# Kernel optimization log

Measured on AMD Instinct MI355X. Metric: run time of the kernel, lower is better.

The kernel has to match this reference:

```python
import jax, jax.numpy as jnp
import numpy as np

D = 512; E = 8; TOPK = 2; F = 2048; H = 4
SF_LEVELS = 4; SF_BASE = 4.0; LN_EPS = 1e-5


def _ln(h, s, b):
    mu = jnp.mean(h, axis=-1, keepdims=True)
    var = jnp.mean((h - mu) ** 2, axis=-1, keepdims=True)
    return (h - mu) / jnp.sqrt(var + LN_EPS) * s + b


def setup_inputs() -> dict:
    key = jax.random.key(0)
    ks = jax.random.split(key, 16)
    sc = 0.02
    inp = {
        "x": jax.random.normal(ks[0], (4, 1024, D), jnp.float32),
        "gate_w": jax.random.normal(ks[1], (D, E), jnp.float32) * sc,
        "gate_b": jnp.zeros((E,), jnp.float32),
        "ln1_s": jnp.ones((E, D), jnp.float32),
        "ln1_b": jnp.zeros((E, D), jnp.float32),
        "ln2_s": jnp.ones((E, D), jnp.float32),
        "ln2_b": jnp.zeros((E, D), jnp.float32),
        "wq": jax.random.normal(ks[2], (E, D, D), jnp.float32) * sc,
        "wk": jax.random.normal(ks[3], (E, D, D), jnp.float32) * sc,
        "wv": jax.random.normal(ks[4], (E, D, D), jnp.float32) * sc,
        "wo": jax.random.normal(ks[5], (E, D, D), jnp.float32) * sc,
        "bq": jnp.zeros((E, D), jnp.float32),
        "bk": jnp.zeros((E, D), jnp.float32),
        "bv": jnp.zeros((E, D), jnp.float32),
        "bo": jnp.zeros((E, D), jnp.float32),
        "w1": jax.random.normal(ks[6], (E, D, F), jnp.float32) * sc,
        "b1": jnp.zeros((E, F), jnp.float32),
        "w2": jax.random.normal(ks[7], (E, F, D), jnp.float32) * sc,
        "b2": jnp.zeros((E, D), jnp.float32),
    }
    return inp


def reference(x, gate_w, gate_b, ln1_s, ln1_b, ln2_s, ln2_b, wq, wk, wv, wo, bq, bk, bv, bo, w1, b1, w2, b2):
    B, S, d = x.shape
    dh = d // H
    # --- SpikingRouter ---
    logits = x @ gate_w + gate_b                       # [B,S,E]
    _, idx = jax.lax.top_k(logits, TOPK)               # [B,S,k]
    in_topk = jnp.sum(jax.nn.one_hot(idx, E, dtype=logits.dtype), axis=-2) > 0
    routing_in = jnp.where(in_topk, jax.nn.relu(logits), 0.0)
    # Scale-and-Fire neuron: multi-level threshold quantization
    mem = routing_in
    rw = jnp.zeros_like(mem)
    for lvl in range(SF_LEVELS):
        thr = SF_BASE / (2.0 ** lvl)
        spk = (mem >= thr).astype(mem.dtype)
        rw = rw + spk * thr
        mem = mem - spk * thr
    # --- all experts (SFormerBlock, post-norm transformer block) ---
    def block(p):
        l1s, l1b, l2s, l2b, Wq, Wk, Wv, Wo, Bq, Bk, Bv, Bo, W1, B1, W2, B2 = p
        q = (x @ Wq + Bq).reshape(B, S, H, dh)
        k = (x @ Wk + Bk).reshape(B, S, H, dh)
        v = (x @ Wv + Bv).reshape(B, S, H, dh)
        scores = jnp.einsum('bqhd,bkhd->bhqk', q, k) / jnp.sqrt(jnp.asarray(dh, x.dtype))
        att = jax.nn.softmax(scores, axis=-1)
        o = jnp.einsum('bhqk,bkhd->bqhd', att, v).reshape(B, S, d) @ Wo + Bo
        h = _ln(x + o, l1s, l1b)
        f = jax.nn.relu(h @ W1 + B1) @ W2 + B2
        return _ln(h + f, l2s, l2b)

    expert_outs = jax.vmap(block)((ln1_s, ln1_b, ln2_s, ln2_b, wq, wk, wv, wo, bq, bk, bv, bo, w1, b1, w2, b2))  # [E,B,S,D]
    final = jnp.einsum('ebsd,bse->bsd', expert_outs, rw)
    return final, logits
```

## Files before the change

kernel.cpp:

```cpp
#include <hip/hip_runtime.h>
#include <hip/hip_bf16.h>
#include <stdint.h>

using u16 = unsigned short;
typedef float floatx4 __attribute__((ext_vector_type(4)));
typedef __bf16 bfv8 __attribute__((ext_vector_type(8)));

#define AS1 __attribute__((address_space(1)))
#define AS3 __attribute__((address_space(3)))

__device__ __forceinline__ u16 f2bf_bits(float f) {
    __hip_bfloat16 h = __float2bfloat16(f);
    u16 u;
    __builtin_memcpy(&u, &h, 2);
    return u;
}
__device__ __forceinline__ float bf_bits2f(u16 u) {
    __hip_bfloat16 h;
    __builtin_memcpy(&h, &u, 2);
    return __bfloat162float(h);
}
__device__ __forceinline__ void gload_lds16(const void* g, void* l) {
    __builtin_amdgcn_global_load_lds((AS1 void*)(uintptr_t)g, (AS3 void*)l, 16, 0, 0);
}

__device__ __forceinline__ void stage64(const u16* __restrict__ Abase, long lda, const long* arow,
                                        const u16* __restrict__ Bb, long ldb, int k0, int tid,
                                        u16* Ad, u16* Bd) {
    #pragma unroll
    for (int j = 0; j < 4; ++j) {
        const int q   = j * 256 + tid;
        const int row = q >> 3;
        const int cg  = (q & 7) ^ (row & 7);
        gload_lds16(Abase + arow[j] * lda + k0 + cg * 8, Ad + q * 8);
        gload_lds16(Bb + (long)row * ldb + k0 + cg * 8, Bd + q * 8);
    }
}
__device__ __forceinline__ void compute64(const u16* Ab, const u16* Bb, int wy, int wx,
                                          int quad, int mrow, floatx4 acc[4][4]) {
    #pragma unroll
    for (int kk = 0; kk < 2; ++kk) {
        bfv8 af[4], bf[4];
        #pragma unroll
        for (int mi = 0; mi < 4; mi++) {
            const int r = wy * 64 + mi * 16 + mrow;
            const int slot = (kk * 4 + quad) ^ (r & 7);
            af[mi] = *(const bfv8*)&Ab[r * 64 + slot * 8];
        }
        #pragma unroll
        for (int ni = 0; ni < 4; ni++) {
            const int r = wx * 64 + ni * 16 + mrow;
            const int slot = (kk * 4 + quad) ^ (r & 7);
            bf[ni] = *(const bfv8*)&Bb[r * 64 + slot * 8];
        }
        #pragma unroll
        for (int mi = 0; mi < 4; mi++)
            #pragma unroll
            for (int ni = 0; ni < 4; ni++)
                acc[mi][ni] = __builtin_amdgcn_mfma_f32_16x16x32_bf16(af[mi], bf[ni], acc[mi][ni], 0, 0, 0);
    }
}

__global__ void cast_bf16_kernel(const float* __restrict__ in, u16* __restrict__ out, int n4) {
    int i = blockIdx.x * blockDim.x + threadIdx.x;
    if (i >= n4) return;
    float4 v = ((const float4*)in)[i];
    ushort4 o;
    o.x = f2bf_bits(v.x); o.y = f2bf_bits(v.y); o.z = f2bf_bits(v.z); o.w = f2bf_bits(v.w);
    ((ushort4*)out)[i] = o;
}

__global__ void transpose_cast_kernel(const float* __restrict__ src, u16* __restrict__ dst,
                                      int R, int C, long sSrc, long sDst) {
    __shared__ float tile[32][33];
    const float* s = src + (long)blockIdx.z * sSrc;
    u16* d = dst + (long)blockIdx.z * sDst;
    int c0 = blockIdx.x * 32, r0 = blockIdx.y * 32;
    int tx = threadIdx.x, ty = threadIdx.y;
    #pragma unroll
    for (int i = 0; i < 4; i++)
        tile[ty + 8*i][tx] = s[(long)(r0 + ty + 8*i) * C + c0 + tx];
    __syncthreads();
    #pragma unroll
    for (int i = 0; i < 4; i++)
        d[(long)(c0 + ty + 8*i) * R + r0 + tx] = f2bf_bits(tile[tx][ty + 8*i]);
}

__global__ void pack_bias_kernel(const float* __restrict__ bq, const float* __restrict__ bk,
                                 const float* __restrict__ bv, float* __restrict__ pb) {
    int i = blockIdx.x * 256 + threadIdx.x;
    const float* s = blockIdx.y == 0 ? bq : (blockIdx.y == 1 ? bk : bv);
    pb[blockIdx.y * 4096 + i] = s[i];
}

__global__ __launch_bounds__(512)
void router_kernel(const float* __restrict__ x, const float* __restrict__ gw,
                   const float* __restrict__ gb, float* __restrict__ rw,
                   float* __restrict__ logits_out) {
    int row = blockIdx.x;
    int w = threadIdx.x >> 6;
    int lane = threadIdx.x & 63;
    const float* xr = x + (long)row * 512;
    float sum = 0.f;
    #pragma unroll
    for (int i = 0; i < 8; i++) {
        int d = lane + 64 * i;
        sum += xr[d] * gw[d * 8 + w];
    }
    #pragma unroll
    for (int o = 32; o; o >>= 1) sum += __shfl_down(sum, o, 64);
    __shared__ float lg[8];
    if (lane == 0) lg[w] = sum + gb[w];
    __syncthreads();
    if (threadIdx.x == 0) {
        float l[8];
        #pragma unroll
        for (int e = 0; e < 8; e++) l[e] = lg[e];
        int i1 = 0;
        for (int e = 1; e < 8; e++) if (l[e] > l[i1]) i1 = e;
        int i2 = -1;
        for (int e = 0; e < 8; e++) { if (e == i1) continue; if (i2 < 0 || l[e] > l[i2]) i2 = e; }
        for (int e = 0; e < 8; e++) {
            float v = (e == i1 || e == i2) ? (l[e] > 0.f ? l[e] : 0.f) : 0.f;
            float r = 0.f, mem = v;
            #pragma unroll
            for (int lvl = 0; lvl < 4; lvl++) {
                float thr = 4.0f / (float)(1 << lvl);
                if (mem >= thr) { r += thr; mem -= thr; }
            }
            rw[(long)row * 8 + e] = r;
            logits_out[(long)row * 8 + e] = l[e];
        }
    }
}

__global__ __launch_bounds__(256)
void build_lists_kernel(const float* __restrict__ rw, int* __restrict__ prix,
                        int* __restrict__ act, int* __restrict__ smap,
                        int* __restrict__ tmap, int* __restrict__ tt, int* __restrict__ pt) {
    int b = blockIdx.x;
    int t = threadIdx.x, wv = t >> 6, lane = t & 63;
    __shared__ int wsum[4];
    __shared__ int base_sh;
    if (t == 0) base_sh = 0;
    __syncthreads();
    for (int e = 0; e < 8; e++) {
        int r0 = b * 1024 + t * 4;
        int f[4], c = 0;
        #pragma unroll
        for (int i = 0; i < 4; i++) {
            f[i] = (rw[(long)(r0 + i) * 8 + e] != 0.f) ? 1 : 0;
            c += f[i];
        }
        int incl = c;
        #pragma unroll
        for (int o = 1; o < 64; o <<= 1) {
            int n = __shfl_up(incl, o, 64);
            if (lane >= o) incl += n;
        }
        if (lane == 63) wsum[wv] = incl;
        __syncthreads();
        int woff = 0;
        #pragma unroll
        for (int k = 0; k < 4; k++) if (k < wv) woff += wsum[k];
        int tot = wsum[0] + wsum[1] + wsum[2] + wsum[3];
        int excl = incl - c + woff;
        int base = base_sh;
        int slot = excl;
        #pragma unroll
        for (int i = 0; i < 4; i++) {
            int r = r0 + i;
            if (f[i]) {
                int ps = base + slot;
                prix[b * 3072 + ps] = r;
                act[b * 3072 + ps] = 1;
                smap[(long)r * 8 + e] = ps;
                slot++;
            } else {
                smap[(long)r * 8 + e] = -1;
            }
        }
        int pad = (tot + 127) & ~127;
        for (int s = tot + t; s < pad; s += 256) {
            prix[b * 3072 + base + s] = b * 1024;
            act[b * 3072 + base + s] = 0;
        }
        for (int k = t; k < (pad >> 7); k += 256)
            tmap[b * 32 + (base >> 7) + k] = e;
        __syncthreads();
        if (t == 0) base_sh = base + pad;
        __syncthreads();
    }
    if (t == 0) {
        tt[b] = base_sh >> 7;
        pt[b] = base_sh;
    }
}

template<bool TRANSC>
__global__ __launch_bounds__(256)
void gemm_dense_kernel(const u16* __restrict__ A,
                       const u16* __restrict__ B, long sB,
                       u16* __restrict__ C, long sC,
                       const float* __restrict__ bias, int K) {
    __shared__ __align__(16) u16 As[2][128 * 64];
    __shared__ __align__(16) u16 Bs[2][128 * 64];
    const int z = blockIdx.z;
    const u16* Bb = B + (long)z * sB + (long)blockIdx.x * 128 * 512;

    const int tid = threadIdx.x;
    const int w = tid >> 6, lane = tid & 63;
    const int wy = w >> 1, wx = w & 1;
    const int quad = lane >> 4, mrow = lane & 15;

    long arow[4];
    #pragma unroll
    for (int j = 0; j < 4; ++j) arow[j] = (long)blockIdx.y * 128 + ((j * 256 + tid) >> 3);

    floatx4 acc[4][4];
    #pragma unroll
    for (int i = 0; i < 4; i++)
        #pragma unroll
        for (int j = 0; j < 4; j++)
            acc[i][j] = floatx4{0.f, 0.f, 0.f, 0.f};

    const int nk = K >> 6;
    stage64(A, 512, arow, Bb, 512, 0, tid, As[0], Bs[0]);
    for (int it = 0; it < nk; ++it) {
        const int cur = it & 1;
        __syncthreads();
        if (it + 1 < nk)
            stage64(A, 512, arow, Bb, 512, (it + 1) << 6, tid, As[1 - cur], Bs[1 - cur]);
        compute64(As[cur], Bs[cur], wy, wx, quad, mrow, acc);
    }

    const float* biasb = bias + (long)z * 512 + blockIdx.x * 128;
    if constexpr (TRANSC) {
        u16* Cb = C + (long)z * sC;
        #pragma unroll
        for (int ni = 0; ni < 4; ni++) {
            const int colt = wx * 64 + ni * 16 + mrow;
            const int n = blockIdx.x * 128 + colt;
            float bv = biasb[colt];
            #pragma unroll
            for (int mi = 0; mi < 4; mi++) {
                #pragma unroll
                for (int r = 0; r < 4; r++) {
                    const int m = blockIdx.y * 128 + wy * 64 + mi * 16 + quad * 4 + r;
                    float v = acc[mi][ni][r] + bv;
                    long addr = ((long)(((m >> 10) << 2) + (n >> 7)) * 128 + (n & 127)) * 1024 + (m & 1023);
                    Cb[addr] = f2bf_bits(v);
                }
            }
        }
    } else {
        u16* Cb = C + (long)z * sC + (long)blockIdx.y * 128 * 512 + blockIdx.x * 128;
        #pragma unroll
        for (int ni = 0; ni < 4; ni++) {
            const int col = wx * 64 + ni * 16 + mrow;
            float bv = biasb[col];
            #pragma unroll
            for (int mi = 0; mi < 4; mi++) {
                #pragma unroll
                for (int r = 0; r < 4; r++) {
                    const int row = wy * 64 + mi * 16 + quad * 4 + r;
                    Cb[(long)row * 512 + col] = f2bf_bits(acc[mi][ni][r] + bv);
                }
            }
        }
    }
}

__global__ __launch_bounds__(256)
void gemm_scores_kernel(const u16* __restrict__ Q, const u16* __restrict__ Km, u16* __restrict__ S,
                        const int* __restrict__ prix, const int* __restrict__ tmap,
                        const int* __restrict__ tt, float alpha) {
    const int b = blockIdx.z >> 2, h = blockIdx.z & 3;
    const int tile = blockIdx.y;
    if (tile >= tt[b]) return;
    const int e = tmap[b * 32 + tile];
    __shared__ __align__(16) u16 As[2][128 * 64];
    __shared__ __align__(16) u16 Bs[2][128 * 64];
    const u16* Abase = Q + (long)e * 4096 * 512 + h * 128;
    const u16* Bb = Km + ((long)e * 4096 + b * 1024 + blockIdx.x * 128) * 512 + h * 128;

    const int tid = threadIdx.x;
    const int w = tid >> 6, lane = tid & 63;
    const int wy = w >> 1, wx = w & 1;
    const int quad = lane >> 4, mrow = lane & 15;

    long arow[4];
    #pragma unroll
    for (int j = 0; j < 4; ++j)
        arow[j] = prix[b * 3072 + tile * 128 + ((j * 256 + tid) >> 3)];

    floatx4 acc[4][4];
    #pragma unroll
    for (int i = 0; i < 4; i++)
        #pragma unroll
        for (int j = 0; j < 4; j++)
            acc[i][j] = floatx4{0.f, 0.f, 0.f, 0.f};

    stage64(Abase, 512, arow, Bb, 512, 0, tid, As[0], Bs[0]);
    for (int it = 0; it < 2; ++it) {
        const int cur = it & 1;
        __syncthreads();
        if (it == 0)
            stage64(Abase, 512, arow, Bb, 512, 64, tid, As[1], Bs[1]);
        compute64(As[cur], Bs[cur], wy, wx, quad, mrow, acc);
    }

    u16* Cb = S + ((long)blockIdx.z * 3072 + tile * 128) * 1024 + blockIdx.x * 128;
    #pragma unroll
    for (int ni = 0; ni < 4; ni++) {
        const int col = wx * 64 + ni * 16 + mrow;
        #pragma unroll
        for (int mi = 0; mi < 4; mi++) {
            #pragma unroll
            for (int r = 0; r < 4; r++) {
                const int row = wy * 64 + mi * 16 + quad * 4 + r;
                Cb[(long)row * 1024 + col] = f2bf_bits(acc[mi][ni][r] * alpha);
            }
        }
    }
}

__global__ __launch_bounds__(256)
void gemm_pv_kernel(const u16* __restrict__ S, const u16* __restrict__ VT, u16* __restrict__ OC,
                    const int* __restrict__ tmap, const int* __restrict__ tt) {
    const int b = blockIdx.z >> 2, h = blockIdx.z & 3;
    const int tile = blockIdx.y;
    if (tile >= tt[b]) return;
    const int e = tmap[b * 32 + tile];
    __shared__ __align__(16) u16 As[2][128 * 64];
    __shared__ __align__(16) u16 Bs[2][128 * 64];
    const u16* Abase = S + ((long)blockIdx.z * 3072 + tile * 128) * 1024;
    const u16* Bb = VT + ((long)e * 16 + blockIdx.z) * 131072;

    const int tid = threadIdx.x;
    const int w = tid >> 6, lane = tid & 63;
    const int wy = w >> 1, wx = w & 1;
    const int quad = lane >> 4, mrow = lane & 15;

    long arow[4];
    #pragma unroll
    for (int j = 0; j < 4; ++j) arow[j] = (j * 256 + tid) >> 3;

    floatx4 acc[4][4];
    #pragma unroll
    for (int i = 0; i < 4; i++)
        #pragma unroll
        for (int j = 0; j < 4; j++)
            acc[i][j] = floatx4{0.f, 0.f, 0.f, 0.f};

    stage64(Abase, 1024, arow, Bb, 1024, 0, tid, As[0], Bs[0]);
    for (int it = 0; it < 16; ++it) {
        const int cur = it & 1;
        __syncthreads();
        if (it + 1 < 16)
            stage64(Abase, 1024, arow, Bb, 1024, (it + 1) << 6, tid, As[1 - cur], Bs[1 - cur]);
        compute64(As[cur], Bs[cur], wy, wx, quad, mrow, acc);
    }

    u16* Cb = OC + ((long)b * 3072 + tile * 128) * 512 + h * 128;
    #pragma unroll
    for (int ni = 0; ni < 4; ni++) {
        const int col = wx * 64 + ni * 16 + mrow;
        #pragma unroll
        for (int mi = 0; mi < 4; mi++) {
            #pragma unroll
            for (int r = 0; r < 4; r++) {
                const int row = wy * 64 + mi * 16 + quad * 4 + r;
                Cb[(long)row * 512 + col] = f2bf_bits(acc[mi][ni][r]);
            }
        }
    }
}

template<bool RELU>
__global__ __launch_bounds__(256)
void gemm_packed_kernel(const u16* __restrict__ A, int lda,
                        const u16* __restrict__ B, int ldb, long sBe,
                        u16* __restrict__ C, int ldc,
                        const float* __restrict__ bias, long sBiasE,
                        const int* __restrict__ tmap, const int* __restrict__ tt, int K) {
    const int b = blockIdx.y / 24, tile = blockIdx.y % 24;
    if (tile >= tt[b]) return;
    const int e = tmap[b * 32 + tile];
    __shared__ __align__(16) u16 As[2][128 * 64];
    __shared__ __align__(16) u16 Bs[2][128 * 64];
    const long rbase = (long)b * 3072 + tile * 128;
    const u16* Ab = A + rbase * lda;
    const u16* Bb = B + (long)e * sBe + (long)blockIdx.x * 128 * ldb;

    const int tid = threadIdx.x;
    const int w = tid >> 6, lane = tid & 63;
    const int wy = w >> 1, wx = w & 1;
    const int quad = lane >> 4, mrow = lane & 15;

    long arow[4];
    #pragma unroll
    for (int j = 0; j < 4; ++j) arow[j] = (j * 256 + tid) >> 3;

    floatx4 acc[4][4];
    #pragma unroll
    for (int i = 0; i < 4; i++)
        #pragma unroll
        for (int j = 0; j < 4; j++)
            acc[i][j] = floatx4{0.f, 0.f, 0.f, 0.f};

    const int nk = K >> 6;
    stage64(Ab, lda, arow, Bb, ldb, 0, tid, As[0], Bs[0]);
    for (int it = 0; it < nk; ++it) {
        const int cur = it & 1;
        __syncthreads();
        if (it + 1 < nk)
            stage64(Ab, lda, arow, Bb, ldb, (it + 1) << 6, tid, As[1 - cur], Bs[1 - cur]);
        compute64(As[cur], Bs[cur], wy, wx, quad, mrow, acc);
    }

    u16* Cb = C + rbase * ldc + (long)blockIdx.x * 128;
    const float* biasb = bias + (long)e * sBiasE + blockIdx.x * 128;
    #pragma unroll
    for (int ni = 0; ni < 4; ni++) {
        const int col = wx * 64 + ni * 16 + mrow;
        float bv = biasb[col];
        #pragma unroll
        for (int mi = 0; mi < 4; mi++) {
            #pragma unroll
            for (int r = 0; r < 4; r++) {
                const int row = wy * 64 + mi * 16 + quad * 4 + r;
                float v = acc[mi][ni][r] + bv;
                if (RELU) v = fmaxf(v, 0.f);
                Cb[(long)row * ldc + col] = f2bf_bits(v);
            }
        }
    }
}

__global__ __launch_bounds__(256)
void softmax_kernel(u16* __restrict__ S, const int* __restrict__ act, const int* __restrict__ pt) {
    int blk = blockIdx.x;
    int pslot = blk % 3072;
    int bh = blk / 3072;
    int b = bh >> 2;
    if (pslot >= pt[b] || !act[b * 3072 + pslot]) return;
    u16* p = S + ((long)bh * 3072 + pslot) * 1024;
    int t = threadIdx.x, w = t >> 6, lane = t & 63;
    float v[4];
    float mx = -1e30f;
    #pragma unroll
    for (int i = 0; i < 4; i++) {
        v[i] = bf_bits2f(p[t + 256 * i]);
        mx = fmaxf(mx, v[i]);
    }
    #pragma unroll
    for (int o = 32; o; o >>= 1) mx = fmaxf(mx, __shfl_down(mx, o, 64));
    __shared__ float red[8];
    if (lane == 0) red[w] = mx;
    __syncthreads();
    mx = fmaxf(fmaxf(red[0], red[1]), fmaxf(red[2], red[3]));
    float sum = 0.f;
    #pragma unroll
    for (int i = 0; i < 4; i++) { v[i] = __expf(v[i] - mx); sum += v[i]; }
    #pragma unroll
    for (int o = 32; o; o >>= 1) sum += __shfl_down(sum, o, 64);
    if (lane == 0) red[4 + w] = sum;
    __syncthreads();
    float inv = 1.f / (red[4] + red[5] + red[6] + red[7]);
    #pragma unroll
    for (int i = 0; i < 4; i++) p[t + 256 * i] = f2bf_bits(v[i] * inv);
}

__global__ __launch_bounds__(128)
void ln1_kernel(const float* __restrict__ x, const u16* __restrict__ tc,
                const int* __restrict__ prix, const int* __restrict__ act,
                const int* __restrict__ tmap, const int* __restrict__ pt,
                const float* __restrict__ s_all, const float* __restrict__ b_all,
                u16* __restrict__ hb) {
    int blk = blockIdx.x;
    int b = blk / 3072, pslot = blk % 3072;
    if (pslot >= pt[b]) return;
    long row = (long)b * 3072 + pslot;
    int tid = threadIdx.x, w = tid >> 6, lane = tid & 63;
    if (!act[row]) {
        *(ushort4*)(hb + row * 512 + tid * 4) = make_ushort4(0, 0, 0, 0);
        return;
    }
    int r = prix[row];
    int e = tmap[b * 32 + (pslot >> 7)];
    float4 xv = *(const float4*)(x + (long)r * 512 + tid * 4);
    ushort4 tu = *(const ushort4*)(tc + row * 512 + tid * 4);
    float v[4] = {xv.x + bf_bits2f(tu.x), xv.y + bf_bits2f(tu.y),
                  xv.z + bf_bits2f(tu.z), xv.w + bf_bits2f(tu.w)};
    float sum = v[0] + v[1] + v[2] + v[3];
    #pragma unroll
    for (int o = 32; o; o >>= 1) sum += __shfl_down(sum, o, 64);
    __shared__ float sh[4];
    if (lane == 0) sh[w] = sum;
    __syncthreads();
    float mu = (sh[0] + sh[1]) * (1.f / 512.f);
    float sq = 0.f;
    #pragma unroll
    for (int j = 0; j < 4; j++) { float d = v[j] - mu; sq += d * d; }
    #pragma unroll
    for (int o = 32; o; o >>= 1) sq += __shfl_down(sq, o, 64);
    if (lane == 0) sh[2 + w] = sq;
    __syncthreads();
    float inv = 1.f / sqrtf((sh[2] + sh[3]) * (1.f / 512.f) + 1e-5f);
    float4 sv = *(const float4*)(s_all + e * 512 + tid * 4);
    float4 bv = *(const float4*)(b_all + e * 512 + tid * 4);
    ushort4 ub;
    ub.x = f2bf_bits((v[0] - mu) * inv * sv.x + bv.x);
    ub.y = f2bf_bits((v[1] - mu) * inv * sv.y + bv.y);
    ub.z = f2bf_bits((v[2] - mu) * inv * sv.z + bv.z);
    ub.w = f2bf_bits((v[3] - mu) * inv * sv.w + bv.w);
    *(ushort4*)(hb + row * 512 + tid * 4) = ub;
}

__global__ __launch_bounds__(128)
void ln2acc_kernel(const u16* __restrict__ hb, const u16* __restrict__ t2,
                   const float* __restrict__ s_all, const float* __restrict__ b_all,
                   const float* __restrict__ rw, const int* __restrict__ smap,
                   float* __restrict__ out) {
    long r = blockIdx.x;
    int b = (int)(r >> 10);
    int tid = threadIdx.x, w = tid >> 6, lane = tid & 63;
    __shared__ float sh[4];
    float4 acc = make_float4(0.f, 0.f, 0.f, 0.f);
    for (int e = 0; e < 8; e++) {
        int ps = smap[r * 8 + e];
        if (ps >= 0) {
            float wgt = rw[r * 8 + e];
            long row = (long)b * 3072 + ps;
            ushort4 hu = *(const ushort4*)(hb + row * 512 + tid * 4);
            ushort4 fu = *(const ushort4*)(t2 + row * 512 + tid * 4);
            float v[4] = {bf_bits2f(hu.x) + bf_bits2f(fu.x), bf_bits2f(hu.y) + bf_bits2f(fu.y),
                          bf_bits2f(hu.z) + bf_bits2f(fu.z), bf_bits2f(hu.w) + bf_bits2f(fu.w)};
            float sum = v[0] + v[1] + v[2] + v[3];
            #pragma unroll
            for (int o = 32; o; o >>= 1) sum += __shfl_down(sum, o, 64);
            if (lane == 0) sh[w] = sum;
            __syncthreads();
            float mu = (sh[0] + sh[1]) * (1.f / 512.f);
            float sq = 0.f;
            #pragma unroll
            for (int j = 0; j < 4; j++) { float d = v[j] - mu; sq += d * d; }
            #pragma unroll
            for (int o = 32; o; o >>= 1) sq += __shfl_down(sq, o, 64);
            if (lane == 0) sh[2 + w] = sq;
            __syncthreads();
            float inv = 1.f / sqrtf((sh[2] + sh[3]) * (1.f / 512.f) + 1e-5f);
            float4 sv = *(const float4*)(s_all + e * 512 + tid * 4);
            float4 bv = *(const float4*)(b_all + e * 512 + tid * 4);
            acc.x += wgt * ((v[0] - mu) * inv * sv.x + bv.x);
            acc.y += wgt * ((v[1] - mu) * inv * sv.y + bv.y);
            acc.z += wgt * ((v[2] - mu) * inv * sv.z + bv.z);
            acc.w += wgt * ((v[3] - mu) * inv * sv.w + bv.w);
            __syncthreads();
        }
    }
    *(float4*)(out + r * 512 + tid * 4) = acc;
}

static const size_t WB_B   = 0;
static const size_t RW_B   = 50331648;
static const size_t PB_B   = 50462720;
static const size_t TT_B   = 50511872;
static const size_t PT_B   = 50511888;
static const size_t TMAP_B = 50511904;
static const size_t PRIX_B = 50512416;
static const size_t ACT_B  = 50561568;
static const size_t SMAP_B = 50610720;
static const size_t XB_B   = 50741792;
static const size_t Q8_B   = 54936096;
static const size_t K8_B   = 88490528;
static const size_t VT_B   = 122044960;
static const size_t S_B    = 155599392;
static const size_t OC_B   = Q8_B;
static const size_t TC_B   = K8_B;
static const size_t HB_B   = Q8_B;
static const size_t MID_B  = S_B;
static const size_t T2_B   = VT_B;

extern "C" void kernel_launch(void* const* d_in, const int* in_sizes, int n_in,
                              void* d_out, int out_size, void* d_ws, size_t ws_size,
                              hipStream_t stream) {
    const float* x      = (const float*)d_in[0];
    const float* gate_w = (const float*)d_in[1];
    const float* gate_b = (const float*)d_in[2];
    const float* ln1_s  = (const float*)d_in[3];
    const float* ln1_b  = (const float*)d_in[4];
    const float* ln2_s  = (const float*)d_in[5];
    const float* ln2_b  = (const float*)d_in[6];
    const float* wq = (const float*)d_in[7];
    const float* wk = (const float*)d_in[8];
    const float* wv = (const float*)d_in[9];
    const float* wo = (const float*)d_in[10];
    const float* bo = (const float*)d_in[14];
    const float* w1 = (const float*)d_in[15];
    const float* b1 = (const float*)d_in[16];
    const float* w2 = (const float*)d_in[17];
    const float* b2 = (const float*)d_in[18];
    float* out = (float*)d_out;

    char* ws = (char*)d_ws;
    u16*   WB   = (u16*)(ws + WB_B);
    float* RW   = (float*)(ws + RW_B);
    float* PB   = (float*)(ws + PB_B);
    int*   TT   = (int*)(ws + TT_B);
    int*   PT   = (int*)(ws + PT_B);
    int*   TMAP = (int*)(ws + TMAP_B);
    int*   PRIX = (int*)(ws + PRIX_B);
    int*   ACT  = (int*)(ws + ACT_B);
    int*   SMAP = (int*)(ws + SMAP_B);
    u16*   XB   = (u16*)(ws + XB_B);
    u16*   Q8   = (u16*)(ws + Q8_B);
    u16*   VT8  = (u16*)(ws + VT_B);
    u16*   S    = (u16*)(ws + S_B);
    u16*   K8   = (u16*)(ws + K8_B);
    u16*   OC   = (u16*)(ws + OC_B);
    u16*   TC   = (u16*)(ws + TC_B);
    u16*   HB   = (u16*)(ws + HB_B);
    u16*   MID  = (u16*)(ws + MID_B);
    u16*   T2   = (u16*)(ws + T2_B);

    cast_bf16_kernel<<<dim3(2048), 256, 0, stream>>>(x, XB, 4096 * 512 / 4);
    transpose_cast_kernel<<<dim3(16,16,8), dim3(32,8), 0, stream>>>(wq, WB + 0,        512,  512,  262144,  262144);
    transpose_cast_kernel<<<dim3(16,16,8), dim3(32,8), 0, stream>>>(wk, WB + 2097152,  512,  512,  262144,  262144);
    transpose_cast_kernel<<<dim3(16,16,8), dim3(32,8), 0, stream>>>(wv, WB + 4194304,  512,  512,  262144,  262144);
    transpose_cast_kernel<<<dim3(16,16,8), dim3(32,8), 0, stream>>>(wo, WB + 6291456,  512,  512,  262144,  262144);
    transpose_cast_kernel<<<dim3(64,16,8), dim3(32,8), 0, stream>>>(w1, WB + 8388608,  512,  2048, 1048576, 1048576);
    transpose_cast_kernel<<<dim3(16,64,8), dim3(32,8), 0, stream>>>(w2, WB + 16777216, 2048, 512,  1048576, 1048576);
    pack_bias_kernel<<<dim3(16,3), 256, 0, stream>>>((const float*)d_in[11], (const float*)d_in[12],
                                                     (const float*)d_in[13], PB);
    router_kernel<<<4096, 512, 0, stream>>>(x, gate_w, gate_b, RW, out + 2097152);
    build_lists_kernel<<<4, 256, 0, stream>>>(RW, PRIX, ACT, SMAP, TMAP, TT, PT);

    const float isq = 0.08838834764831845f;

    gemm_dense_kernel<false><<<dim3(4,32,16), 256, 0, stream>>>(
        XB, WB, 262144, Q8, 2097152, PB, 512);
    gemm_dense_kernel<true><<<dim3(4,32,8), 256, 0, stream>>>(
        XB, WB + 4194304, 262144, VT8, 2097152, PB + 8192, 512);

    gemm_scores_kernel<<<dim3(8,24,16), 256, 0, stream>>>(
        Q8, K8, S, PRIX, TMAP, TT, isq);
    softmax_kernel<<<49152, 256, 0, stream>>>(S, ACT, PT);
    gemm_pv_kernel<<<dim3(1,24,16), 256, 0, stream>>>(S, VT8, OC, TMAP, TT);

    gemm_packed_kernel<false><<<dim3(4,96), 256, 0, stream>>>(
        OC, 512, WB + 6291456, 512, 262144, TC, 512, bo, 512, TMAP, TT, 512);
    ln1_kernel<<<12288, 128, 0, stream>>>(x, TC, PRIX, ACT, TMAP, PT, ln1_s, ln1_b, HB);
    gemm_packed_kernel<true><<<dim3(16,96), 256, 0, stream>>>(
        HB, 512, WB + 8388608, 512, 1048576, MID, 2048, b1, 2048, TMAP, TT, 512);
    gemm_packed_kernel<false><<<dim3(4,96), 256, 0, stream>>>(
        MID, 2048, WB + 16777216, 2048, 1048576, T2, 512, b2, 512, TMAP, TT, 2048);
    ln2acc_kernel<<<4096, 128, 0, stream>>>(HB, T2, ln2_s, ln2_b, RW, SMAP, out);
}
```

Before: 502.9 us.

## Fuse softmax into score GEMM epilogue and compute Q only for routed tokens

Removes the standalone softmax kernel. The scores GEMM now applies exp in its epilogue and writes per-tile row partial sums, and the PV GEMM normalises its output by the reciprocal of the summed partials. Q projection changes from a dense GEMM over all tokens for every expert to a gathered packed GEMM over only the routed rows. The weight transpose launches and the bias pack are also merged into fewer kernels. Exp is taken without max subtraction, which risks overflow for large scores, and a new partial-sum buffer is added to the workspace.

Measured after the change: 477.0 us. 5.1% less time.

```diff
diff --git a/kernel.cpp b/kernel.cpp
--- a/kernel.cpp
+++ b/kernel.cpp
@@ -61,7 +61,15 @@
     }
 }
 
-__global__ void cast_bf16_kernel(const float* __restrict__ in, u16* __restrict__ out, int n4) {
+__global__ void cast_bf16_kernel(const float* __restrict__ in, u16* __restrict__ out, int n4,
+                                 const float* __restrict__ bq, const float* __restrict__ bk,
+                                 const float* __restrict__ bv, float* __restrict__ pb) {
+    if (blockIdx.x >= 2048) {
+        int j = (blockIdx.x - 2048) * 256 + threadIdx.x;
+        const float* s = j < 4096 ? bq : (j < 8192 ? bk : bv);
+        pb[j] = s[j & 4095];
+        return;
+    }
     int i = blockIdx.x * blockDim.x + threadIdx.x;
     if (i >= n4) return;
     float4 v = ((const float4*)in)[i];
@@ -86,11 +94,22 @@
         d[(long)(c0 + ty + 8*i) * R + r0 + tx] = f2bf_bits(tile[tx][ty + 8*i]);
 }
 
-__global__ void pack_bias_kernel(const float* __restrict__ bq, const float* __restrict__ bk,
-                                 const float* __restrict__ bv, float* __restrict__ pb) {
-    int i = blockIdx.x * 256 + threadIdx.x;
-    const float* s = blockIdx.y == 0 ? bq : (blockIdx.y == 1 ? bk : bv);
-    pb[blockIdx.y * 4096 + i] = s[i];
+__global__ void transpose_cast4_kernel(const float* __restrict__ w0, const float* __restrict__ w1p,
+                                       const float* __restrict__ w2p, const float* __restrict__ w3p,
+                                       u16* __restrict__ dst) {
+    __shared__ float tile[32][33];
+    int z = blockIdx.z;
+    const float* s = (z < 8 ? w0 : z < 16 ? w1p : z < 24 ? w2p : w3p) + (long)(z & 7) * 262144;
+    u16* d = dst + (long)z * 262144;
+    int c0 = blockIdx.x * 32, r0 = blockIdx.y * 32;
+    int tx = threadIdx.x, ty = threadIdx.y;
+    #pragma unroll
+    for (int i = 0; i < 4; i++)
+        tile[ty + 8*i][tx] = s[(long)(r0 + ty + 8*i) * 512 + c0 + tx];
+    __syncthreads();
+    #pragma unroll
+    for (int i = 0; i < 4; i++)
+        d[(long)(c0 + ty + 8*i) * 512 + r0 + tx] = f2bf_bits(tile[tx][ty + 8*i]);
 }
 
 __global__ __launch_bounds__(512)
@@ -272,16 +291,17 @@
 }
 
 __global__ __launch_bounds__(256)
-void gemm_scores_kernel(const u16* __restrict__ Q, const u16* __restrict__ Km, u16* __restrict__ S,
-                        const int* __restrict__ prix, const int* __restrict__ tmap,
-                        const int* __restrict__ tt, float alpha) {
+void gemm_scores_kernel(const u16* __restrict__ QP, const u16* __restrict__ Km, u16* __restrict__ S,
+                        const int* __restrict__ tmap, const int* __restrict__ tt,
+                        float* __restrict__ psum, float alpha) {
     const int b = blockIdx.z >> 2, h = blockIdx.z & 3;
     const int tile = blockIdx.y;
     if (tile >= tt[b]) return;
     const int e = tmap[b * 32 + tile];
     __shared__ __align__(16) u16 As[2][128 * 64];
     __shared__ __align__(16) u16 Bs[2][128 * 64];
-    const u16* Abase = Q + (long)e * 4096 * 512 + h * 128;
+    __shared__ float psh[2][128];
+    const u16* Abase = QP + (long)b * 3072 * 512 + h * 128;
     const u16* Bb = Km + ((long)e * 4096 + b * 1024 + blockIdx.x * 128) * 512 + h * 128;
 
     const int tid = threadIdx.x;
@@ -292,7 +312,7 @@
     long arow[4];
     #pragma unroll
     for (int j = 0; j < 4; ++j)
-        arow[j] = prix[b * 3072 + tile * 128 + ((j * 256 + tid) >> 3)];
+        arow[j] = tile * 128 + ((j * 256 + tid) >> 3);
 
     floatx4 acc[4][4];
     #pragma unroll
@@ -310,6 +330,28 @@
         compute64(As[cur], Bs[cur], wy, wx, quad, mrow, acc);
     }
 
+    #pragma unroll
+    for (int mi = 0; mi < 4; mi++) {
+        #pragma unroll
+        for (int r = 0; r < 4; r++) {
+            float s = 0.f;
+            #pragma unroll
+            for (int ni = 0; ni < 4; ni++) {
+                float p = __expf(acc[mi][ni][r] * alpha);
+                acc[mi][ni][r] = p;
+                s += p;
+            }
+            #pragma unroll
+            for (int o = 1; o < 16; o <<= 1) s += __shfl_xor(s, o, 64);
+            if (mrow == 0) psh[wx][wy * 64 + mi * 16 + quad * 4 + r] = s;
+        }
+    }
+    __syncthreads();
+    if (tid < 128) {
+        long prow = (long)blockIdx.z * 3072 + tile * 128 + tid;
+        psum[prow * 8 + blockIdx.x] = psh[0][tid] + psh[1][tid];
+    }
+
     u16* Cb = S + ((long)blockIdx.z * 3072 + tile * 128) * 1024 + blockIdx.x * 128;
     #pragma unroll
     for (int ni = 0; ni < 4; ni++) {
@@ -319,7 +361,7 @@
             #pragma unroll
             for (int r = 0; r < 4; r++) {
                 const int row = wy * 64 + mi * 16 + quad * 4 + r;
-                Cb[(long)row * 1024 + col] = f2bf_bits(acc[mi][ni][r] * alpha);
+                Cb[(long)row * 1024 + col] = f2bf_bits(acc[mi][ni][r]);
             }
         }
     }
@@ -327,13 +369,15 @@
 
 __global__ __launch_bounds__(256)
 void gemm_pv_kernel(const u16* __restrict__ S, const u16* __restrict__ VT, u16* __restrict__ OC,
-                    const int* __restrict__ tmap, const int* __restrict__ tt) {
+                    const int* __restrict__ tmap, const int* __restrict__ tt,
+                    const float* __restrict__ psum) {
     const int b = blockIdx.z >> 2, h = blockIdx.z & 3;
     const int tile = blockIdx.y;
     if (tile >= tt[b]) return;
     const int e = tmap[b * 32 + tile];
     __shared__ __align__(16) u16 As[2][128 * 64];
     __shared__ __align__(16) u16 Bs[2][128 * 64];
+    __shared__ float invs[128];
     const u16* Abase = S + ((long)blockIdx.z * 3072 + tile * 128) * 1024;
     const u16* Bb = VT + ((long)e * 16 + blockIdx.z) * 131072;
 
@@ -341,6 +385,14 @@
     const int w = tid >> 6, lane = tid & 63;
     const int wy = w >> 1, wx = w & 1;
     const int quad = lane >> 4, mrow = lane & 15;
+
+    if (tid < 128) {
+        const float* ps = psum + ((long)blockIdx.z * 3072 + tile * 128 + tid) * 8;
+        float s = 0.f;
+        #pragma unroll
+        for (int i = 0; i < 8; i++) s += ps[i];
+        invs[tid] = 1.f / s;
+    }
 
     long arow[4];
     #pragma unroll
@@ -371,26 +423,27 @@
             #pragma unroll
             for (int r = 0; r < 4; r++) {
                 const int row = wy * 64 + mi * 16 + quad * 4 + r;
-                Cb[(long)row * 512 + col] = f2bf_bits(acc[mi][ni][r]);
-            }
-        }
-    }
-}
-
-template<bool RELU>
+                Cb[(long)row * 512 + col] = f2bf_bits(acc[mi][ni][r] * invs[row]);
+            }
+        }
+    }
+}
+
+template<bool RELU, bool GATHER>
 __global__ __launch_bounds__(256)
 void gemm_packed_kernel(const u16* __restrict__ A, int lda,
                         const u16* __restrict__ B, int ldb, long sBe,
                         u16* __restrict__ C, int ldc,
                         const float* __restrict__ bias, long sBiasE,
-                        const int* __restrict__ tmap, const int* __restrict__ tt, int K) {
+                        const int* __restrict__ tmap, const int* __restrict__ tt, int K,
+                        const int* __restrict__ prix) {
     const int b = blockIdx.y / 24, tile = blockIdx.y % 24;
     if (tile >= tt[b]) return;
     const int e = tmap[b * 32 + tile];
     __shared__ __align__(16) u16 As[2][128 * 64];
     __shared__ __align__(16) u16 Bs[2][128 * 64];
     const long rbase = (long)b * 3072 + tile * 128;
-    const u16* Ab = A + rbase * lda;
+    const u16* Ab = GATHER ? A : A + rbase * lda;
     const u16* Bb = B + (long)e * sBe + (long)blockIdx.x * 128 * ldb;
 
     const int tid = threadIdx.x;
@@ -400,7 +453,10 @@
 
     long arow[4];
     #pragma unroll
-    for (int j = 0; j < 4; ++j) arow[j] = (j * 256 + tid) >> 3;
+    for (int j = 0; j < 4; ++j) {
+        const int lr = (j * 256 + tid) >> 3;
+        arow[j] = GATHER ? (long)prix[b * 3072 + tile * 128 + lr] : (long)lr;
+    }
 
     floatx4 acc[4][4];
     #pragma unroll
@@ -436,40 +492,6 @@
             }
         }
     }
-}
-
-__global__ __launch_bounds__(256)
-void softmax_kernel(u16* __restrict__ S, const int* __restrict__ act, const int* __restrict__ pt) {
-    int blk = blockIdx.x;
-    int pslot = blk % 3072;
-    int bh = blk / 3072;
-    int b = bh >> 2;
-    if (pslot >= pt[b] || !act[b * 3072 + pslot]) return;
-    u16* p = S + ((long)bh * 3072 + pslot) * 1024;
-    int t = threadIdx.x, w = t >> 6, lane = t & 63;
-    float v[4];
-    float mx = -1e30f;
-    #pragma unroll
-    for (int i = 0; i < 4; i++) {
-        v[i] = bf_bits2f(p[t + 256 * i]);
-        mx = fmaxf(mx, v[i]);
-    }
-    #pragma unroll
-    for (int o = 32; o; o >>= 1) mx = fmaxf(mx, __shfl_down(mx, o, 64));
-    __shared__ float red[8];
-    if (lane == 0) red[w] = mx;
-    __syncthreads();
-    mx = fmaxf(fmaxf(red[0], red[1]), fmaxf(red[2], red[3]));
-    float sum = 0.f;
-    #pragma unroll
-    for (int i = 0; i < 4; i++) { v[i] = __expf(v[i] - mx); sum += v[i]; }
-    #pragma unroll
-    for (int o = 32; o; o >>= 1) sum += __shfl_down(sum, o, 64);
-    if (lane == 0) red[4 + w] = sum;
-    __syncthreads();
-    float inv = 1.f / (red[4] + red[5] + red[6] + red[7]);
-    #pragma unroll
-    for (int i = 0; i < 4; i++) p[t + 256 * i] = f2bf_bits(v[i] * inv);
 }
 
 __global__ __launch_bounds__(128)
@@ -577,6 +599,7 @@
 static const size_t K8_B   = 88490528;
 static const size_t VT_B   = 122044960;
 static const size_t S_B    = 155599392;
+static const size_t PSUM_B = 256262688;
 static const size_t OC_B   = Q8_B;
 static const size_t TC_B   = K8_B;
 static const size_t HB_B   = Q8_B;
@@ -615,46 +638,45 @@
     int*   ACT  = (int*)(ws + ACT_B);
     int*   SMAP = (int*)(ws + SMAP_B);
     u16*   XB   = (u16*)(ws + XB_B);
-    u16*   Q8   = (u16*)(ws + Q8_B);
+    u16*   QP   = (u16*)(ws + Q8_B);
+    u16*   K8   = (u16*)(ws + K8_B);
     u16*   VT8  = (u16*)(ws + VT_B);
     u16*   S    = (u16*)(ws + S_B);
-    u16*   K8   = (u16*)(ws + K8_B);
+    float* PSUM = (float*)(ws + PSUM_B);
     u16*   OC   = (u16*)(ws + OC_B);
     u16*   TC   = (u16*)(ws + TC_B);
     u16*   HB   = (u16*)(ws + HB_B);
     u16*   MID  = (u16*)(ws + MID_B);
     u16*   T2   = (u16*)(ws + T2_B);
 
-    cast_bf16_kernel<<<dim3(2048), 256, 0, stream>>>(x, XB, 4096 * 512 / 4);
-    transpose_cast_kernel<<<dim3(16,16,8), dim3(32,8), 0, stream>>>(wq, WB + 0,        512,  512,  262144,  262144);
-    transpose_cast_kernel<<<dim3(16,16,8), dim3(32,8), 0, stream>>>(wk, WB + 2097152,  512,  512,  262144,  262144);
-    transpose_cast_kernel<<<dim3(16,16,8), dim3(32,8), 0, stream>>>(wv, WB + 4194304,  512,  512,  262144,  262144);
-    transpose_cast_kernel<<<dim3(16,16,8), dim3(32,8), 0, stream>>>(wo, WB + 6291456,  512,  512,  262144,  262144);
+    cast_bf16_kernel<<<dim3(2096), 256, 0, stream>>>(x, XB, 4096 * 512 / 4,
+                                                     (const float*)d_in[11], (const float*)d_in[12],
+                                                     (const float*)d_in[13], PB);
+    transpose_cast4_kernel<<<dim3(16,16,32), dim3(32,8), 0, stream>>>(wq, wk, wv, wo, WB);
     transpose_cast_kernel<<<dim3(64,16,8), dim3(32,8), 0, stream>>>(w1, WB + 8388608,  512,  2048, 1048576, 1048576);
     transpose_cast_kernel<<<dim3(16,64,8), dim3(32,8), 0, stream>>>(w2, WB + 16777216, 2048, 512,  1048576, 1048576);
-    pack_bias_kernel<<<dim3(16,3), 256, 0, stream>>>((const float*)d_in[11], (const float*)d_in[12],
-                                                     (const float*)d_in[13], PB);
     router_kernel<<<4096, 512, 0, stream>>>(x, gate_w, gate_b, RW, out + 2097152);
     build_lists_kernel<<<4, 256, 0, stream>>>(RW, PRIX, ACT, SMAP, TMAP, TT, PT);
 
     const float isq = 0.08838834764831845f;
 
-    gemm_dense_kernel<false><<<dim3(4,32,16), 256, 0, stream>>>(
-        XB, WB, 262144, Q8, 2097152, PB, 512);
+    gemm_dense_kernel<false><<<dim3(4,32,8), 256, 0, stream>>>(
+        XB, WB + 2097152, 262144, K8, 2097152, PB + 4096, 512);
     gemm_dense_kernel<true><<<dim3(4,32,8), 256, 0, stream>>>(
         XB, WB + 4194304, 262144, VT8, 2097152, PB + 8192, 512);
+    gemm_packed_kernel<false, true><<<dim3(4,96), 256, 0, stream>>>(
+        XB, 512, WB, 512, 262144, QP, 512, PB, 512, TMAP, TT, 512, PRIX);
 
     gemm_scores_kernel<<<dim3(8,24,16), 256, 0, stream>>>(
-        Q8, K8, S, PRIX, TMAP, TT, isq);
-    softmax_kernel<<<49152, 256, 0, stream>>>(S, ACT, PT);
-    gemm_pv_kernel<<<dim3(1,24,16), 256, 0, stream>>>(S, VT8, OC, TMAP, TT);
-
-    gemm_packed_kernel<false><<<dim3(4,96), 256, 0, stream>>>(
-        OC, 512, WB + 6291456, 512, 262144, TC, 512, bo, 512, TMAP, TT, 512);
+        QP, K8, S, TMAP, TT, PSUM, isq);
+    gemm_pv_kernel<<<dim3(1,24,16), 256, 0, stream>>>(S, VT8, OC, TMAP, TT, PSUM);
+
+    gemm_packed_kernel<false, false><<<dim3(4,96), 256, 0, stream>>>(
+        OC, 512, WB + 6291456, 512, 262144, TC, 512, bo, 512, TMAP, TT, 512, nullptr);
     ln1_kernel<<<12288, 128, 0, stream>>>(x, TC, PRIX, ACT, TMAP, PT, ln1_s, ln1_b, HB);
-    gemm_packed_kernel<true><<<dim3(16,96), 256, 0, stream>>>(
-        HB, 512, WB + 8388608, 512, 1048576, MID, 2048, b1, 2048, TMAP, TT, 512);
-    gemm_packed_kernel<false><<<dim3(4,96), 256, 0, stream>>>(
-        MID, 2048, WB + 16777216, 2048, 1048576, T2, 512, b2, 512, TMAP, TT, 2048);
+    gemm_packed_kernel<true, false><<<dim3(16,96), 256, 0, stream>>>(
+        HB, 512, WB + 8388608, 512, 1048576, MID, 2048, b1, 2048, TMAP, TT, 512, nullptr);
+    gemm_packed_kernel<false, false><<<dim3(4,96), 256, 0, stream>>>(
+        MID, 2048, WB + 16777216, 2048, 1048576, T2, 512, b2, 512, TMAP, TT, 2048, nullptr);
     ln2acc_kernel<<<4096, 128, 0, stream>>>(HB, T2, ln2_s, ln2_b, RW, SMAP, out);
 }
```
